# Performance work log

Hardware: AMD Instinct MI355X
Metric: run time of the kernel (lower is better)

The kernel has to match this reference:

```python
import jax, jax.numpy as jnp
import numpy as np

EPS = 1e-6


def setup_inputs() -> dict:
    key = jax.random.key(0)
    k1, k2, k3 = jax.random.split(key, 3)
    B, H, L, D = 1, 16, 1024, 64
    return {
        "q": jax.random.normal(k1, (B, H, L, D), dtype=jnp.float32),
        "k": jax.random.normal(k2, (B, H, L, D), dtype=jnp.float32),
        "v": jax.random.normal(k3, (B, H, L, D), dtype=jnp.float32),
    }


def reference(q, k, v):
    bsz, head_num, tgt_len, dim = q.shape
    src_len = k.shape[2]
    m = max(src_len, tgt_len)

    # flatten batch*heads: [N, L, D]
    q = jax.nn.relu(q.reshape(-1, tgt_len, dim))
    k = jax.nn.relu(k.reshape(-1, src_len, dim))
    v = v.reshape(-1, src_len, dim)

    # cosFormer re-weighting index: pi/2 * (1..m) / m, shape [1, m, 1]
    idx = (np.pi / 2) * jnp.arange(1, m + 1, dtype=q.dtype).reshape(1, -1, 1) / m
    sin_w = jnp.sin(idx)
    cos_w = jnp.cos(idx)

    # feature-mapped q/k: [N, L, 2D]
    q_ = jnp.concatenate([q * sin_w[:, :tgt_len, :], q * cos_w[:, :tgt_len, :]], axis=-1)
    k_ = jnp.concatenate([k * sin_w[:, :src_len, :], k * cos_w[:, :src_len, :]], axis=-1)

    # causal linear attention via cumulative outer products
    kv_ = jnp.einsum("nld,nlm->nldm", k_, v)          # [N, L, 2D, D]
    kv_cum = jnp.cumsum(kv_, axis=1)
    qkv = jnp.einsum("nld,nldm->nlm", q_, kv_cum)      # [N, L, D]

    k_cum = jnp.cumsum(k_, axis=1)                      # [N, L, 2D]
    denom = jnp.clip(jnp.einsum("nld,nld->nl", q_, k_cum), EPS, None)

    out = qkv / denom[..., None]
    return out.reshape(bsz, head_num, tgt_len, dim)
```

## Files before the change

kernel.cpp:

```cpp
#include <hip/hip_runtime.h>

namespace {
constexpr int Hh = 16;
constexpr int Ll = 1024;
constexpr int Dd = 64;
constexpr int Cc = 64;
constexpr int NCHUNK = Ll / Cc;
constexpr float PI_HALF = 1.5707963267948966f;
constexpr float EPSV = 1e-6f;
constexpr int KV_ELEMS = 128 * 64;
constexpr size_t KV_TOTAL_E = (size_t)Hh * NCHUNK * KV_ELEMS;
}

typedef __attribute__((ext_vector_type(8))) short short8;
typedef __attribute__((ext_vector_type(4))) float floatx4;

__device__ __forceinline__ unsigned short f2bf(float x) {
    unsigned int u = __float_as_uint(x);
    unsigned int r = u + 0x7fffu + ((u >> 16) & 1u);
    return (unsigned short)(r >> 16);
}
__device__ __forceinline__ float bf2f(unsigned short b) {
    return __uint_as_float(((unsigned int)b) << 16);
}

__global__ __launch_bounds__(256)
void cf_sums(const float* __restrict__ kin, const float* __restrict__ vin,
             unsigned short* __restrict__ wskv, unsigned short* __restrict__ wsks) {
    const int c = blockIdx.x, h = blockIdx.y;
    const int tid = threadIdx.x;
    constexpr int S1 = 72, SC = 136;
    __shared__ unsigned short Ak[128 * S1];
    __shared__ unsigned short Bv1[80 * S1];
    __shared__ unsigned short Cst[64 * SC];
    __shared__ unsigned short Ks[128];

    const size_t gbase = ((size_t)h * Ll + (size_t)c * Cc) * Dd;
    const float4* k4 = (const float4*)(kin + gbase);
    const float4* v4 = (const float4*)(vin + gbase);
    #pragma unroll
    for (int i = 0; i < 4; ++i) {
        int e4 = i * 256 + tid;
        int j = e4 >> 4, d4 = (e4 & 15) * 4;
        float th = PI_HALF * (float)(c * Cc + j + 1) * (1.0f / (float)Ll);
        float sj, cj; __sincosf(th, &sj, &cj);
        float4 kx = k4[e4];
        float r0 = fmaxf(kx.x, 0.f), r1 = fmaxf(kx.y, 0.f);
        float r2 = fmaxf(kx.z, 0.f), r3 = fmaxf(kx.w, 0.f);
        Ak[(d4 + 0) * S1 + j] = f2bf(r0 * sj);
        Ak[(d4 + 1) * S1 + j] = f2bf(r1 * sj);
        Ak[(d4 + 2) * S1 + j] = f2bf(r2 * sj);
        Ak[(d4 + 3) * S1 + j] = f2bf(r3 * sj);
        Ak[(64 + d4 + 0) * S1 + j] = f2bf(r0 * cj);
        Ak[(64 + d4 + 1) * S1 + j] = f2bf(r1 * cj);
        Ak[(64 + d4 + 2) * S1 + j] = f2bf(r2 * cj);
        Ak[(64 + d4 + 3) * S1 + j] = f2bf(r3 * cj);
        float4 vx = v4[e4];
        Bv1[(d4 + 0) * S1 + j] = f2bf(vx.x);
        Bv1[(d4 + 1) * S1 + j] = f2bf(vx.y);
        Bv1[(d4 + 2) * S1 + j] = f2bf(vx.z);
        Bv1[(d4 + 3) * S1 + j] = f2bf(vx.w);
    }
    if (tid < 64) Bv1[64 * S1 + tid] = 0x3F80;
    if (tid >= 64 && tid < 72) Bv1[64 * S1 + tid] = 0;
    #pragma unroll
    for (int i = 0; i < 3; ++i) {
        int z = i * 256 + tid;
        if (z < 540) ((unsigned int*)Bv1)[(65 * S1) / 2 + z] = 0u;
    }
    __syncthreads();

    const int wave = tid >> 6, lane = tid & 63;
    const int lrow = lane & 15, quad = lane >> 4;
    #pragma unroll
    for (int t = 0; t < 2; ++t) {
        const int ft = wave * 2 + t;
        short8 af[2];
        #pragma unroll
        for (int ks = 0; ks < 2; ++ks)
            af[ks] = *(const short8*)&Ak[(ft * 16 + lrow) * S1 + ks * 32 + quad * 8];
        #pragma unroll
        for (int nt = 0; nt < 5; ++nt) {
            floatx4 acc = {0.f, 0.f, 0.f, 0.f};
            #pragma unroll
            for (int ks = 0; ks < 2; ++ks) {
                short8 bf = *(const short8*)&Bv1[(nt * 16 + lrow) * S1 + ks * 32 + quad * 8];
                acc = __builtin_amdgcn_mfma_f32_16x16x32_bf16(af[ks], bf, acc, 0, 0, 0);
            }
            ushort4 pk = make_ushort4(f2bf(acc[0]), f2bf(acc[1]), f2bf(acc[2]), f2bf(acc[3]));
            if (nt < 4) {
                *(ushort4*)&Cst[(nt * 16 + lrow) * SC + ft * 16 + quad * 4] = pk;
            } else if (lrow == 0) {
                *(ushort4*)&Ks[ft * 16 + quad * 4] = pk;
            }
        }
    }
    __syncthreads();

    unsigned short* kvout = wskv + (size_t)(h * NCHUNK + c) * KV_ELEMS;
    #pragma unroll
    for (int i = 0; i < 4; ++i) {
        int idx = i * 256 + tid;
        int row = idx >> 4, c8 = (idx & 15) * 8;
        *(uint4*)(kvout + row * 128 + c8) = *(const uint4*)&Cst[row * SC + c8];
    }
    if (tid < 16)
        *(uint4*)(wsks + (size_t)(h * NCHUNK + c) * 128 + tid * 8) =
            *(const uint4*)&Ks[tid * 8];
}

__global__ __launch_bounds__(256)
void cf_scan(unsigned short* __restrict__ wskv, unsigned short* __restrict__ wsks) {
    const int bx = blockIdx.x, h = blockIdx.y;
    const int tid = threadIdx.x;
    if (bx < 32) {
        unsigned short* p = wskv + (size_t)h * NCHUNK * KV_ELEMS + bx * 256 + tid;
        float run = 0.f;
        #pragma unroll
        for (int cc = 0; cc < NCHUNK; ++cc) {
            float v = bf2f(p[(size_t)cc * KV_ELEMS]);
            p[(size_t)cc * KV_ELEMS] = f2bf(run);
            run += v;
        }
    } else if (tid < 128) {
        unsigned short* p = wsks + (size_t)h * NCHUNK * 128 + tid;
        float run = 0.f;
        #pragma unroll
        for (int cc = 0; cc < NCHUNK; ++cc) {
            float v = bf2f(p[cc * 128]);
            p[cc * 128] = f2bf(run);
            run += v;
        }
    }
}

__global__ __launch_bounds__(256)
void cf_out(const float* __restrict__ qin, const float* __restrict__ kin,
            const float* __restrict__ vin,
            const unsigned short* __restrict__ wskv,
            const unsigned short* __restrict__ wsks,
            float* __restrict__ out) {
    const int c = blockIdx.x, h = blockIdx.y;
    const int tid = threadIdx.x;
    constexpr int SA = 200, SB = 136, SV = 200;
    __shared__ unsigned short Aq[64 * SA];
    __shared__ unsigned short Bk[80 * SB];
    __shared__ unsigned short Bv[64 * SV];

    const size_t gbase = ((size_t)h * Ll + (size_t)c * Cc) * Dd;
    const float4* q4 = (const float4*)(qin + gbase);
    const float4* k4 = (const float4*)(kin + gbase);
    const float4* v4 = (const float4*)(vin + gbase);
    #pragma unroll
    for (int i = 0; i < 4; ++i) {
        int e4 = i * 256 + tid;
        int j = e4 >> 4, d4 = (e4 & 15) * 4;
        float th = PI_HALF * (float)(c * Cc + j + 1) * (1.0f / (float)Ll);
        float sj, cj; __sincosf(th, &sj, &cj);
        float4 qv = q4[e4];
        float q0 = fmaxf(qv.x, 0.f), q1 = fmaxf(qv.y, 0.f);
        float q2 = fmaxf(qv.z, 0.f), q3 = fmaxf(qv.w, 0.f);
        *(ushort4*)&Aq[j * SA + 64 + d4] =
            make_ushort4(f2bf(q0 * sj), f2bf(q1 * sj), f2bf(q2 * sj), f2bf(q3 * sj));
        *(ushort4*)&Aq[j * SA + 128 + d4] =
            make_ushort4(f2bf(q0 * cj), f2bf(q1 * cj), f2bf(q2 * cj), f2bf(q3 * cj));
        float4 kx = k4[e4];
        float k0 = fmaxf(kx.x, 0.f), k1 = fmaxf(kx.y, 0.f);
        float k2 = fmaxf(kx.z, 0.f), k3 = fmaxf(kx.w, 0.f);
        *(ushort4*)&Bk[j * SB + d4] =
            make_ushort4(f2bf(k0 * sj), f2bf(k1 * sj), f2bf(k2 * sj), f2bf(k3 * sj));
        *(ushort4*)&Bk[j * SB + 64 + d4] =
            make_ushort4(f2bf(k0 * cj), f2bf(k1 * cj), f2bf(k2 * cj), f2bf(k3 * cj));
        float4 vx = v4[e4];
        Bv[(d4 + 0) * SV + j] = f2bf(vx.x);
        Bv[(d4 + 1) * SV + j] = f2bf(vx.y);
        Bv[(d4 + 2) * SV + j] = f2bf(vx.z);
        Bv[(d4 + 3) * SV + j] = f2bf(vx.w);
    }
    const uint4* s4 = (const uint4*)(wskv + (size_t)(h * NCHUNK + c) * KV_ELEMS);
    #pragma unroll
    for (int i = 0; i < 4; ++i) {
        int idx = i * 256 + tid;
        int d = idx >> 4, f8 = (idx & 15) * 8;
        *(uint4*)&Bv[d * SV + 64 + f8] = s4[idx];
    }
    if (tid < 16)
        *(uint4*)&Bk[64 * SB + tid * 8] =
            ((const uint4*)(wsks + (size_t)(h * NCHUNK + c) * 128))[tid];
    #pragma unroll
    for (int i = 0; i < 4; ++i) {
        int z = i * 256 + tid;
        if (z < 1020) ((unsigned int*)Bk)[(65 * SB) / 2 + z] = 0u;
    }
    __syncthreads();

    const int wave = tid >> 6, lane = tid & 63;
    const int lrow = lane & 15, quad = lane >> 4;
    const int l0 = wave * 16;
    const int arow = (l0 + lrow) * SA;

    short8 a1[4];
    #pragma unroll
    for (int ks = 0; ks < 4; ++ks)
        a1[ks] = *(const short8*)&Aq[arow + 64 + ks * 32 + quad * 8];
    floatx4 rs = {0.f, 0.f, 0.f, 0.f};
    #pragma unroll
    for (int nt = 0; nt < 5; ++nt) {
        floatx4 acc = {0.f, 0.f, 0.f, 0.f};
        #pragma unroll
        for (int ks = 0; ks < 4; ++ks) {
            short8 bf = *(const short8*)&Bk[(nt * 16 + lrow) * SB + ks * 32 + quad * 8];
            acc = __builtin_amdgcn_mfma_f32_16x16x32_bf16(a1[ks], bf, acc, 0, 0, 0);
        }
        if (nt < 4) {
            int j = nt * 16 + lrow;
            #pragma unroll
            for (int r = 0; r < 4; ++r) {
                int l = l0 + quad * 4 + r;
                float m = (j <= l) ? acc[r] : 0.f;
                acc[r] = m;
                Aq[l * SA + j] = f2bf(m);
            }
        }
        rs += acc;
    }
    #pragma unroll
    for (int m = 1; m <= 8; m <<= 1) {
        rs[0] += __shfl_xor(rs[0], m);
        rs[1] += __shfl_xor(rs[1], m);
        rs[2] += __shfl_xor(rs[2], m);
        rs[3] += __shfl_xor(rs[3], m);
    }
    float inv[4];
    #pragma unroll
    for (int r = 0; r < 4; ++r) inv[r] = 1.0f / fmaxf(rs[r], EPSV);

    __syncthreads();

    short8 s0 = *(const short8*)&Aq[arow + 0 * 32 + quad * 8];
    short8 s1 = *(const short8*)&Aq[arow + 1 * 32 + quad * 8];
    #pragma unroll
    for (int nt = 0; nt < 4; ++nt) {
        const int brow = (nt * 16 + lrow) * SV;
        floatx4 acc = {0.f, 0.f, 0.f, 0.f};
        short8 b0 = *(const short8*)&Bv[brow + 0 * 32 + quad * 8];
        acc = __builtin_amdgcn_mfma_f32_16x16x32_bf16(s0, b0, acc, 0, 0, 0);
        short8 b1 = *(const short8*)&Bv[brow + 1 * 32 + quad * 8];
        acc = __builtin_amdgcn_mfma_f32_16x16x32_bf16(s1, b1, acc, 0, 0, 0);
        #pragma unroll
        for (int ks = 2; ks < 6; ++ks) {
            short8 bf = *(const short8*)&Bv[brow + ks * 32 + quad * 8];
            acc = __builtin_amdgcn_mfma_f32_16x16x32_bf16(a1[ks - 2], bf, acc, 0, 0, 0);
        }
        #pragma unroll
        for (int r = 0; r < 4; ++r) {
            int l = l0 + quad * 4 + r;
            out[gbase + (size_t)l * Dd + nt * 16 + lrow] = acc[r] * inv[r];
        }
    }
}

extern "C" void kernel_launch(void* const* d_in, const int* in_sizes, int n_in,
                              void* d_out, int out_size, void* d_ws, size_t ws_size,
                              hipStream_t stream) {
    const float* q = (const float*)d_in[0];
    const float* k = (const float*)d_in[1];
    const float* v = (const float*)d_in[2];
    float* out = (float*)d_out;
    unsigned short* wskv = (unsigned short*)d_ws;
    unsigned short* wsks = wskv + KV_TOTAL_E;
    dim3 grid(NCHUNK, Hh);
    cf_sums<<<grid, 256, 0, stream>>>(k, v, wskv, wsks);
    cf_scan<<<dim3(33, Hh), 256, 0, stream>>>(wskv, wsks);
    cf_out<<<grid, 256, 0, stream>>>(q, k, v, wskv, wsks, out);
}
```

Before: 77.01 us.

## Fuse chunk sums, scan and output into one kernel recomputing prefix state

Replaces the three-kernel pipeline (per-chunk KV sums, cross-chunk scan, output) with a single kernel. Each block recomputes the prefix KV state itself by accumulating MFMA outer products over all earlier chunks, with register prefetch of the next chunk and an XOR-swizzled LDS layout. This removes two launches and the bf16 workspace round-trips. In exchange the redundant work grows quadratically with chunk index, so the blocks for late chunks do up to 15 serial iterations and the load is unbalanced.

```diff
diff --git a/kernel.cpp b/kernel.cpp
--- a/kernel.cpp
+++ b/kernel.cpp
@@ -8,8 +8,10 @@
 constexpr int NCHUNK = Ll / Cc;
 constexpr float PI_HALF = 1.5707963267948966f;
 constexpr float EPSV = 1e-6f;
-constexpr int KV_ELEMS = 128 * 64;
-constexpr size_t KV_TOTAL_E = (size_t)Hh * NCHUNK * KV_ELEMS;
+constexpr int S1 = 72;
+constexpr int SA = 200;
+constexpr int SB = 136;
+constexpr int SV = 200;
 }
 
 typedef __attribute__((ext_vector_type(8))) short short8;
@@ -20,209 +22,188 @@
     unsigned int r = u + 0x7fffu + ((u >> 16) & 1u);
     return (unsigned short)(r >> 16);
 }
-__device__ __forceinline__ float bf2f(unsigned short b) {
-    return __uint_as_float(((unsigned int)b) << 16);
+
+__device__ __forceinline__ int sw1(int row, int j) {
+    return (j & 7) | ((((j >> 3) ^ (row >> 3)) & 7) << 3);
 }
 
 __global__ __launch_bounds__(256)
-void cf_sums(const float* __restrict__ kin, const float* __restrict__ vin,
-             unsigned short* __restrict__ wskv, unsigned short* __restrict__ wsks) {
+void cf_fused(const float* __restrict__ qin, const float* __restrict__ kin,
+              const float* __restrict__ vin, float* __restrict__ out) {
     const int c = blockIdx.x, h = blockIdx.y;
     const int tid = threadIdx.x;
-    constexpr int S1 = 72, SC = 136;
     __shared__ unsigned short Ak[128 * S1];
     __shared__ unsigned short Bv1[80 * S1];
-    __shared__ unsigned short Cst[64 * SC];
-    __shared__ unsigned short Ks[128];
-
-    const size_t gbase = ((size_t)h * Ll + (size_t)c * Cc) * Dd;
+    __shared__ unsigned short Aq[64 * SA];
+    __shared__ unsigned short Bk[80 * SB];
+    __shared__ unsigned short Bv[64 * SV];
+
+    const int wave = tid >> 6, lane = tid & 63;
+    const int lrow = lane & 15, quad = lane >> 4;
+
+    const size_t hbase = (size_t)h * Ll * Dd;
+    const size_t gbase = hbase + (size_t)c * Cc * Dd;
+
+    const float4* q4 = (const float4*)(qin + gbase);
     const float4* k4 = (const float4*)(kin + gbase);
     const float4* v4 = (const float4*)(vin + gbase);
+    float4 oq[4], ok[4], ov[4], pk[4], pv[4];
+    #pragma unroll
+    for (int i = 0; i < 4; ++i) {
+        oq[i] = q4[i * 256 + tid];
+        ok[i] = k4[i * 256 + tid];
+        ov[i] = v4[i * 256 + tid];
+    }
+    if (c > 0) {
+        const float4* kp = (const float4*)(kin + hbase);
+        const float4* vp = (const float4*)(vin + hbase);
+        #pragma unroll
+        for (int i = 0; i < 4; ++i) {
+            pk[i] = kp[i * 256 + tid];
+            pv[i] = vp[i * 256 + tid];
+        }
+    }
+
     #pragma unroll
     for (int i = 0; i < 4; ++i) {
         int e4 = i * 256 + tid;
         int j = e4 >> 4, d4 = (e4 & 15) * 4;
         float th = PI_HALF * (float)(c * Cc + j + 1) * (1.0f / (float)Ll);
-        float sj, cj; __sincosf(th, &sj, &cj);
-        float4 kx = k4[e4];
-        float r0 = fmaxf(kx.x, 0.f), r1 = fmaxf(kx.y, 0.f);
-        float r2 = fmaxf(kx.z, 0.f), r3 = fmaxf(kx.w, 0.f);
-        Ak[(d4 + 0) * S1 + j] = f2bf(r0 * sj);
-        Ak[(d4 + 1) * S1 + j] = f2bf(r1 * sj);
-        Ak[(d4 + 2) * S1 + j] = f2bf(r2 * sj);
-        Ak[(d4 + 3) * S1 + j] = f2bf(r3 * sj);
-        Ak[(64 + d4 + 0) * S1 + j] = f2bf(r0 * cj);
-        Ak[(64 + d4 + 1) * S1 + j] = f2bf(r1 * cj);
-        Ak[(64 + d4 + 2) * S1 + j] = f2bf(r2 * cj);
-        Ak[(64 + d4 + 3) * S1 + j] = f2bf(r3 * cj);
-        float4 vx = v4[e4];
-        Bv1[(d4 + 0) * S1 + j] = f2bf(vx.x);
-        Bv1[(d4 + 1) * S1 + j] = f2bf(vx.y);
-        Bv1[(d4 + 2) * S1 + j] = f2bf(vx.z);
-        Bv1[(d4 + 3) * S1 + j] = f2bf(vx.w);
-    }
-    if (tid < 64) Bv1[64 * S1 + tid] = 0x3F80;
-    if (tid >= 64 && tid < 72) Bv1[64 * S1 + tid] = 0;
-    #pragma unroll
-    for (int i = 0; i < 3; ++i) {
-        int z = i * 256 + tid;
-        if (z < 540) ((unsigned int*)Bv1)[(65 * S1) / 2 + z] = 0u;
-    }
-    __syncthreads();
-
-    const int wave = tid >> 6, lane = tid & 63;
-    const int lrow = lane & 15, quad = lane >> 4;
-    #pragma unroll
-    for (int t = 0; t < 2; ++t) {
-        const int ft = wave * 2 + t;
-        short8 af[2];
-        #pragma unroll
-        for (int ks = 0; ks < 2; ++ks)
-            af[ks] = *(const short8*)&Ak[(ft * 16 + lrow) * S1 + ks * 32 + quad * 8];
-        #pragma unroll
-        for (int nt = 0; nt < 5; ++nt) {
-            floatx4 acc = {0.f, 0.f, 0.f, 0.f};
-            #pragma unroll
-            for (int ks = 0; ks < 2; ++ks) {
-                short8 bf = *(const short8*)&Bv1[(nt * 16 + lrow) * S1 + ks * 32 + quad * 8];
-                acc = __builtin_amdgcn_mfma_f32_16x16x32_bf16(af[ks], bf, acc, 0, 0, 0);
-            }
-            ushort4 pk = make_ushort4(f2bf(acc[0]), f2bf(acc[1]), f2bf(acc[2]), f2bf(acc[3]));
-            if (nt < 4) {
-                *(ushort4*)&Cst[(nt * 16 + lrow) * SC + ft * 16 + quad * 4] = pk;
-            } else if (lrow == 0) {
-                *(ushort4*)&Ks[ft * 16 + quad * 4] = pk;
-            }
-        }
-    }
-    __syncthreads();
-
-    unsigned short* kvout = wskv + (size_t)(h * NCHUNK + c) * KV_ELEMS;
-    #pragma unroll
-    for (int i = 0; i < 4; ++i) {
-        int idx = i * 256 + tid;
-        int row = idx >> 4, c8 = (idx & 15) * 8;
-        *(uint4*)(kvout + row * 128 + c8) = *(const uint4*)&Cst[row * SC + c8];
-    }
-    if (tid < 16)
-        *(uint4*)(wsks + (size_t)(h * NCHUNK + c) * 128 + tid * 8) =
-            *(const uint4*)&Ks[tid * 8];
-}
-
-__global__ __launch_bounds__(256)
-void cf_scan(unsigned short* __restrict__ wskv, unsigned short* __restrict__ wsks) {
-    const int bx = blockIdx.x, h = blockIdx.y;
-    const int tid = threadIdx.x;
-    if (bx < 32) {
-        unsigned short* p = wskv + (size_t)h * NCHUNK * KV_ELEMS + bx * 256 + tid;
-        float run = 0.f;
-        #pragma unroll
-        for (int cc = 0; cc < NCHUNK; ++cc) {
-            float v = bf2f(p[(size_t)cc * KV_ELEMS]);
-            p[(size_t)cc * KV_ELEMS] = f2bf(run);
-            run += v;
-        }
-    } else if (tid < 128) {
-        unsigned short* p = wsks + (size_t)h * NCHUNK * 128 + tid;
-        float run = 0.f;
-        #pragma unroll
-        for (int cc = 0; cc < NCHUNK; ++cc) {
-            float v = bf2f(p[cc * 128]);
-            p[cc * 128] = f2bf(run);
-            run += v;
-        }
-    }
-}
-
-__global__ __launch_bounds__(256)
-void cf_out(const float* __restrict__ qin, const float* __restrict__ kin,
-            const float* __restrict__ vin,
-            const unsigned short* __restrict__ wskv,
-            const unsigned short* __restrict__ wsks,
-            float* __restrict__ out) {
-    const int c = blockIdx.x, h = blockIdx.y;
-    const int tid = threadIdx.x;
-    constexpr int SA = 200, SB = 136, SV = 200;
-    __shared__ unsigned short Aq[64 * SA];
-    __shared__ unsigned short Bk[80 * SB];
-    __shared__ unsigned short Bv[64 * SV];
-
-    const size_t gbase = ((size_t)h * Ll + (size_t)c * Cc) * Dd;
-    const float4* q4 = (const float4*)(qin + gbase);
-    const float4* k4 = (const float4*)(kin + gbase);
-    const float4* v4 = (const float4*)(vin + gbase);
-    #pragma unroll
-    for (int i = 0; i < 4; ++i) {
-        int e4 = i * 256 + tid;
-        int j = e4 >> 4, d4 = (e4 & 15) * 4;
-        float th = PI_HALF * (float)(c * Cc + j + 1) * (1.0f / (float)Ll);
-        float sj, cj; __sincosf(th, &sj, &cj);
-        float4 qv = q4[e4];
-        float q0 = fmaxf(qv.x, 0.f), q1 = fmaxf(qv.y, 0.f);
-        float q2 = fmaxf(qv.z, 0.f), q3 = fmaxf(qv.w, 0.f);
+        float sj, cj;
+        __sincosf(th, &sj, &cj);
+        float q0 = fmaxf(oq[i].x, 0.f), q1 = fmaxf(oq[i].y, 0.f);
+        float q2 = fmaxf(oq[i].z, 0.f), q3 = fmaxf(oq[i].w, 0.f);
         *(ushort4*)&Aq[j * SA + 64 + d4] =
             make_ushort4(f2bf(q0 * sj), f2bf(q1 * sj), f2bf(q2 * sj), f2bf(q3 * sj));
         *(ushort4*)&Aq[j * SA + 128 + d4] =
             make_ushort4(f2bf(q0 * cj), f2bf(q1 * cj), f2bf(q2 * cj), f2bf(q3 * cj));
-        float4 kx = k4[e4];
-        float k0 = fmaxf(kx.x, 0.f), k1 = fmaxf(kx.y, 0.f);
-        float k2 = fmaxf(kx.z, 0.f), k3 = fmaxf(kx.w, 0.f);
+        float k0 = fmaxf(ok[i].x, 0.f), k1 = fmaxf(ok[i].y, 0.f);
+        float k2 = fmaxf(ok[i].z, 0.f), k3 = fmaxf(ok[i].w, 0.f);
         *(ushort4*)&Bk[j * SB + d4] =
             make_ushort4(f2bf(k0 * sj), f2bf(k1 * sj), f2bf(k2 * sj), f2bf(k3 * sj));
         *(ushort4*)&Bk[j * SB + 64 + d4] =
             make_ushort4(f2bf(k0 * cj), f2bf(k1 * cj), f2bf(k2 * cj), f2bf(k3 * cj));
-        float4 vx = v4[e4];
-        Bv[(d4 + 0) * SV + j] = f2bf(vx.x);
-        Bv[(d4 + 1) * SV + j] = f2bf(vx.y);
-        Bv[(d4 + 2) * SV + j] = f2bf(vx.z);
-        Bv[(d4 + 3) * SV + j] = f2bf(vx.w);
-    }
-    const uint4* s4 = (const uint4*)(wskv + (size_t)(h * NCHUNK + c) * KV_ELEMS);
-    #pragma unroll
-    for (int i = 0; i < 4; ++i) {
-        int idx = i * 256 + tid;
-        int d = idx >> 4, f8 = (idx & 15) * 8;
-        *(uint4*)&Bv[d * SV + 64 + f8] = s4[idx];
-    }
-    if (tid < 16)
-        *(uint4*)&Bk[64 * SB + tid * 8] =
-            ((const uint4*)(wsks + (size_t)(h * NCHUNK + c) * 128))[tid];
+        Bv[(d4 + 0) * SV + j] = f2bf(ov[i].x);
+        Bv[(d4 + 1) * SV + j] = f2bf(ov[i].y);
+        Bv[(d4 + 2) * SV + j] = f2bf(ov[i].z);
+        Bv[(d4 + 3) * SV + j] = f2bf(ov[i].w);
+    }
     #pragma unroll
     for (int i = 0; i < 4; ++i) {
         int z = i * 256 + tid;
-        if (z < 1020) ((unsigned int*)Bk)[(65 * SB) / 2 + z] = 0u;
+        if (z < (15 * SB) / 2) ((unsigned int*)Bk)[(65 * SB) / 2 + z] = 0u;
+    }
+    if (tid < 64) Bv1[64 * S1 + tid] = 0x3F80;
+    if (tid >= 64 && tid < S1) Bv1[64 * S1 + tid] = 0;
+    #pragma unroll
+    for (int i = 0; i < 3; ++i) {
+        int z = i * 256 + tid;
+        if (z < (15 * S1) / 2) ((unsigned int*)Bv1)[(65 * S1) / 2 + z] = 0u;
+    }
+
+    floatx4 acc[2][5];
+    #pragma unroll
+    for (int t = 0; t < 2; ++t)
+        #pragma unroll
+        for (int nt = 0; nt < 5; ++nt)
+            acc[t][nt] = (floatx4){0.f, 0.f, 0.f, 0.f};
+
+    for (int cp = 0; cp < c; ++cp) {
+        #pragma unroll
+        for (int i = 0; i < 4; ++i) {
+            int e4 = i * 256 + tid;
+            int j = e4 >> 4, d4 = (e4 & 15) * 4;
+            float th = PI_HALF * (float)(cp * Cc + j + 1) * (1.0f / (float)Ll);
+            float sj, cj;
+            __sincosf(th, &sj, &cj);
+            float r0 = fmaxf(pk[i].x, 0.f), r1 = fmaxf(pk[i].y, 0.f);
+            float r2 = fmaxf(pk[i].z, 0.f), r3 = fmaxf(pk[i].w, 0.f);
+            int col = sw1(d4, j);
+            Ak[(d4 + 0) * S1 + col] = f2bf(r0 * sj);
+            Ak[(d4 + 1) * S1 + col] = f2bf(r1 * sj);
+            Ak[(d4 + 2) * S1 + col] = f2bf(r2 * sj);
+            Ak[(d4 + 3) * S1 + col] = f2bf(r3 * sj);
+            Ak[(64 + d4 + 0) * S1 + col] = f2bf(r0 * cj);
+            Ak[(64 + d4 + 1) * S1 + col] = f2bf(r1 * cj);
+            Ak[(64 + d4 + 2) * S1 + col] = f2bf(r2 * cj);
+            Ak[(64 + d4 + 3) * S1 + col] = f2bf(r3 * cj);
+            Bv1[(d4 + 0) * S1 + col] = f2bf(pv[i].x);
+            Bv1[(d4 + 1) * S1 + col] = f2bf(pv[i].y);
+            Bv1[(d4 + 2) * S1 + col] = f2bf(pv[i].z);
+            Bv1[(d4 + 3) * S1 + col] = f2bf(pv[i].w);
+        }
+        __syncthreads();
+        if (cp + 1 < c) {
+            const float4* kp = (const float4*)(kin + hbase + (size_t)(cp + 1) * Cc * Dd);
+            const float4* vp = (const float4*)(vin + hbase + (size_t)(cp + 1) * Cc * Dd);
+            #pragma unroll
+            for (int i = 0; i < 4; ++i) {
+                pk[i] = kp[i * 256 + tid];
+                pv[i] = vp[i * 256 + tid];
+            }
+        }
+        #pragma unroll
+        for (int t = 0; t < 2; ++t) {
+            int fr = (wave * 2 + t) * 16 + lrow;
+            int keyA = (fr >> 3) & 7;
+            short8 a0 = *(const short8*)&Ak[fr * S1 + ((quad ^ keyA) << 3)];
+            short8 a1 = *(const short8*)&Ak[fr * S1 + (((4 + quad) ^ keyA) << 3)];
+            #pragma unroll
+            for (int nt = 0; nt < 5; ++nt) {
+                int nr = nt * 16 + lrow;
+                int keyB = (nr >> 3) & 7;
+                short8 b0 = *(const short8*)&Bv1[nr * S1 + ((quad ^ keyB) << 3)];
+                short8 b1 = *(const short8*)&Bv1[nr * S1 + (((4 + quad) ^ keyB) << 3)];
+                acc[t][nt] = __builtin_amdgcn_mfma_f32_16x16x32_bf16(a0, b0, acc[t][nt], 0, 0, 0);
+                acc[t][nt] = __builtin_amdgcn_mfma_f32_16x16x32_bf16(a1, b1, acc[t][nt], 0, 0, 0);
+            }
+        }
+        __syncthreads();
+    }
+
+    #pragma unroll
+    for (int t = 0; t < 2; ++t) {
+        int fb = wave * 32 + t * 16 + quad * 4;
+        #pragma unroll
+        for (int nt = 0; nt < 4; ++nt) {
+            int d = nt * 16 + lrow;
+            *(ushort4*)&Bv[d * SV + 64 + fb] =
+                make_ushort4(f2bf(acc[t][nt][0]), f2bf(acc[t][nt][1]),
+                             f2bf(acc[t][nt][2]), f2bf(acc[t][nt][3]));
+        }
+        if (lrow == 0)
+            *(ushort4*)&Bk[64 * SB + fb] =
+                make_ushort4(f2bf(acc[t][4][0]), f2bf(acc[t][4][1]),
+                             f2bf(acc[t][4][2]), f2bf(acc[t][4][3]));
     }
     __syncthreads();
 
-    const int wave = tid >> 6, lane = tid & 63;
-    const int lrow = lane & 15, quad = lane >> 4;
     const int l0 = wave * 16;
     const int arow = (l0 + lrow) * SA;
-
-    short8 a1[4];
+    short8 a1f[4];
     #pragma unroll
     for (int ks = 0; ks < 4; ++ks)
-        a1[ks] = *(const short8*)&Aq[arow + 64 + ks * 32 + quad * 8];
+        a1f[ks] = *(const short8*)&Aq[arow + 64 + ks * 32 + quad * 8];
     floatx4 rs = {0.f, 0.f, 0.f, 0.f};
     #pragma unroll
     for (int nt = 0; nt < 5; ++nt) {
-        floatx4 acc = {0.f, 0.f, 0.f, 0.f};
+        floatx4 s = {0.f, 0.f, 0.f, 0.f};
         #pragma unroll
         for (int ks = 0; ks < 4; ++ks) {
             short8 bf = *(const short8*)&Bk[(nt * 16 + lrow) * SB + ks * 32 + quad * 8];
-            acc = __builtin_amdgcn_mfma_f32_16x16x32_bf16(a1[ks], bf, acc, 0, 0, 0);
+            s = __builtin_amdgcn_mfma_f32_16x16x32_bf16(a1f[ks], bf, s, 0, 0, 0);
         }
         if (nt < 4) {
             int j = nt * 16 + lrow;
             #pragma unroll
             for (int r = 0; r < 4; ++r) {
                 int l = l0 + quad * 4 + r;
-                float m = (j <= l) ? acc[r] : 0.f;
-                acc[r] = m;
+                float m = (j <= l) ? s[r] : 0.f;
+                s[r] = m;
                 Aq[l * SA + j] = f2bf(m);
             }
         }
-        rs += acc;
+        rs += s;
     }
     #pragma unroll
     for (int m = 1; m <= 8; m <<= 1) {
@@ -237,25 +218,25 @@
 
     __syncthreads();
 
-    short8 s0 = *(const short8*)&Aq[arow + 0 * 32 + quad * 8];
-    short8 s1 = *(const short8*)&Aq[arow + 1 * 32 + quad * 8];
+    short8 s0 = *(const short8*)&Aq[arow + quad * 8];
+    short8 s1 = *(const short8*)&Aq[arow + 32 + quad * 8];
     #pragma unroll
     for (int nt = 0; nt < 4; ++nt) {
         const int brow = (nt * 16 + lrow) * SV;
-        floatx4 acc = {0.f, 0.f, 0.f, 0.f};
-        short8 b0 = *(const short8*)&Bv[brow + 0 * 32 + quad * 8];
-        acc = __builtin_amdgcn_mfma_f32_16x16x32_bf16(s0, b0, acc, 0, 0, 0);
-        short8 b1 = *(const short8*)&Bv[brow + 1 * 32 + quad * 8];
-        acc = __builtin_amdgcn_mfma_f32_16x16x32_bf16(s1, b1, acc, 0, 0, 0);
+        floatx4 a2 = {0.f, 0.f, 0.f, 0.f};
+        a2 = __builtin_amdgcn_mfma_f32_16x16x32_bf16(
+                 s0, *(const short8*)&Bv[brow + quad * 8], a2, 0, 0, 0);
+        a2 = __builtin_amdgcn_mfma_f32_16x16x32_bf16(
+                 s1, *(const short8*)&Bv[brow + 32 + quad * 8], a2, 0, 0, 0);
         #pragma unroll
         for (int ks = 2; ks < 6; ++ks) {
             short8 bf = *(const short8*)&Bv[brow + ks * 32 + quad * 8];
-            acc = __builtin_amdgcn_mfma_f32_16x16x32_bf16(a1[ks - 2], bf, acc, 0, 0, 0);
+            a2 = __builtin_amdgcn_mfma_f32_16x16x32_bf16(a1f[ks - 2], bf, a2, 0, 0, 0);
         }
         #pragma unroll
         for (int r = 0; r < 4; ++r) {
             int l = l0 + quad * 4 + r;
-            out[gbase + (size_t)l * Dd + nt * 16 + lrow] = acc[r] * inv[r];
+            out[gbase + (size_t)l * Dd + nt * 16 + lrow] = a2[r] * inv[r];
         }
     }
 }
@@ -267,10 +248,6 @@
     const float* k = (const float*)d_in[1];
     const float* v = (const float*)d_in[2];
     float* out = (float*)d_out;
-    unsigned short* wskv = (unsigned short*)d_ws;
-    unsigned short* wsks = wskv + KV_TOTAL_E;
-    dim3 grid(NCHUNK, Hh);
-    cf_sums<<<grid, 256, 0, stream>>>(k, v, wskv, wsks);
-    cf_scan<<<dim3(33, Hh), 256, 0, stream>>>(wskv, wsks);
-    cf_out<<<grid, 256, 0, stream>>>(q, k, v, wskv, wsks, out);
-}
+    (void)d_ws; (void)ws_size;
+    cf_fused<<<dim3(NCHUNK, Hh), 256, 0, stream>>>(q, k, v, out);
+}
```

New measurement: 87.19 us. 13.2% more time.
